# Kernel tuning notes

Hardware: AMD Instinct MI355X
Metric: run time of the kernel (lower is better)

Reference implementation:

```python
import jax, jax.numpy as jnp
import numpy as np


def _gcn_conv(x, src, dst, deg_inv_sqrt, W, b):
    # PyG GCNConv: h = x @ W; out = sum_{j->i} norm_ij * h_j  (+ bias)
    # src/dst already include self-loops; deg_inv_sqrt computed with self-loops.
    h = x @ W                                   # [N, F_out]
    norm = deg_inv_sqrt[src] * deg_inv_sqrt[dst]  # [E']
    msgs = h[src] * norm[:, None]               # [E', F_out] gather + scale
    out = jax.ops.segment_sum(msgs, dst, num_segments=x.shape[0])
    return out + b


def setup_inputs() -> dict:
    key = jax.random.key(0)
    k1, k2, k3, k4, k5 = jax.random.split(key, 5)
    N, E = 100000, 3200000
    in_c, hid, out_c = 256, 32, 128
    x = jax.random.normal(k1, (N, in_c), dtype=jnp.float32)
    edge_index = jax.random.randint(k2, (2, E), 0, N, dtype=jnp.int64)
    # Glorot-init weights, zero bias (PyG GCNConv defaults)
    W1 = jax.random.normal(k3, (in_c, hid), dtype=jnp.float32) * (2.0 / (in_c + hid)) ** 0.5
    b1 = jnp.zeros((hid,), dtype=jnp.float32)
    W2 = jax.random.normal(k4, (hid, out_c), dtype=jnp.float32) * (2.0 / (hid + out_c)) ** 0.5
    b2 = jnp.zeros((out_c,), dtype=jnp.float32)
    return {"x": x, "edge_index": edge_index, "W1": W1, "b1": b1, "W2": W2, "b2": b2}


def reference(x, edge_index, W1, b1, W2, b2):
    N = x.shape[0]
    # Add self-loops once; shared by both layers.
    loop = jnp.arange(N, dtype=edge_index.dtype)
    src = jnp.concatenate([edge_index[0], loop])
    dst = jnp.concatenate([edge_index[1], loop])
    deg = jax.ops.segment_sum(jnp.ones_like(dst, dtype=x.dtype), dst, num_segments=N)
    deg_inv_sqrt = jnp.where(deg > 0, jax.lax.rsqrt(deg), 0.0)

    h = _gcn_conv(x, src, dst, deg_inv_sqrt, W1, b1)
    h = jax.nn.relu(h)
    out = _gcn_conv(h, src, dst, deg_inv_sqrt, W2, b2)
    return out
```

## Files before the change

kernel.cpp:

```cpp
#include <hip/hip_runtime.h>

#define BSH 7
#define BNODES 128
#define SCHUNK 8192
#define MAXBUCK 800

static __device__ __forceinline__ float frelu(float v){ return v > 0.f ? v : 0.f; }

typedef __attribute__((ext_vector_type(8))) short bf16x8;
typedef __attribute__((ext_vector_type(4))) float f32x4;

static __device__ __forceinline__ unsigned short bf16_trunc(float f){
    return (unsigned short)(__builtin_bit_cast(unsigned int, f) >> 16);
}
static __device__ __forceinline__ float bf16_back(unsigned short h){
    return __builtin_bit_cast(float, ((unsigned int)h) << 16);
}

__global__ void detect_kernel(const unsigned int* __restrict__ e, int* __restrict__ flag){
    __shared__ int odd_nz;
    if (threadIdx.x == 0) odd_nz = 0;
    __syncthreads();
    int local = 0;
    for (int i = threadIdx.x; i < 512; i += blockDim.x){
        if (e[2*i + 1] != 0u) local = 1;
    }
    if (local) atomicOr(&odd_nz, 1);
    __syncthreads();
    if (threadIdx.x == 0) *flag = (odd_nz == 0) ? 1 : 0;
}

static __device__ __forceinline__ int load_idx(const void* eidx, int flg, long long pos){
    if (flg) return (int)((const long long*)eidx)[pos];
    return ((const int*)eidx)[pos];
}

__global__ void w1cvt_kernel(const float* __restrict__ W1,
        unsigned short* __restrict__ Whi, unsigned short* __restrict__ Wlo){
    int i = blockIdx.x * 256 + threadIdx.x;
    if (i < 8192){
        int k = i >> 5, c = i & 31;
        float f = W1[i];
        unsigned short h = bf16_trunc(f);
        unsigned short l = bf16_trunc(f - bf16_back(h));
        Whi[c * 256 + k] = h;
        Wlo[c * 256 + k] = l;
    }
}

__global__ __launch_bounds__(512) void buckcount_kernel(const void* __restrict__ eidx,
        const int* __restrict__ flag, int* __restrict__ bcnt, int E, int nbuck){
    __shared__ int h[MAXBUCK];
    int tid = threadIdx.x;
    int flg = *flag;
    for (int i = tid; i < nbuck; i += 512) h[i] = 0;
    __syncthreads();
    long long c0 = (long long)blockIdx.x * SCHUNK;
    int cnt = (int)min((long long)SCHUNK, (long long)E - c0);
    for (int i = tid; i < cnt; i += 512)
        atomicAdd(&h[load_idx(eidx, flg, (long long)E + c0 + i) >> BSH], 1);
    __syncthreads();
    for (int i = tid; i < nbuck; i += 512)
        if (h[i]) atomicAdd(&bcnt[i], h[i]);
}

__global__ void bucket_scan_kernel(const int* __restrict__ bcnt, int* __restrict__ boff,
                                   int* __restrict__ bcursor, int nbuck){
    __shared__ int sums[1024];
    int tid = threadIdx.x;
    int s = (tid < nbuck) ? bcnt[tid] : 0;
    sums[tid] = s;
    __syncthreads();
    for (int off = 1; off < 1024; off <<= 1){
        int t = (tid >= off) ? sums[tid - off] : 0;
        __syncthreads();
        sums[tid] += t;
        __syncthreads();
    }
    if (tid < nbuck){
        int pfx = sums[tid] - s;
        boff[tid]    = pfx;
        bcursor[tid] = pfx;
    }
    if (tid == 0) boff[nbuck] = sums[1023];
}

__global__ __launch_bounds__(512) void binned_scatter_kernel(
        const void* __restrict__ eidx, const int* __restrict__ flag,
        int* __restrict__ bcursor, unsigned int* __restrict__ bpk, int E, int nbuck){
    __shared__ int hist[MAXBUCK];
    __shared__ int base[MAXBUCK];
    __shared__ unsigned short rank[SCHUNK];
    int tid = threadIdx.x;
    int flg = *flag;
    long long c0 = (long long)blockIdx.x * SCHUNK;
    int cnt = (int)min((long long)SCHUNK, (long long)E - c0);
    for (int i = tid; i < nbuck; i += 512) hist[i] = 0;
    __syncthreads();
    for (int i = tid; i < cnt; i += 512){
        int dst = load_idx(eidx, flg, (long long)E + c0 + i);
        rank[i] = (unsigned short)atomicAdd(&hist[dst >> BSH], 1);
    }
    __syncthreads();
    for (int i = tid; i < nbuck; i += 512){
        int h = hist[i];
        base[i] = h ? atomicAdd(&bcursor[i], h) : 0;
    }
    __syncthreads();
    for (int i = tid; i < cnt; i += 512){
        int src = load_idx(eidx, flg, c0 + i);
        int dst = load_idx(eidx, flg, (long long)E + c0 + i);
        unsigned int local = (unsigned int)(dst & (BNODES - 1));
        bpk[base[dst >> BSH] + (int)rank[i]] = (local << 24) | (unsigned int)src;
    }
}

__global__ __launch_bounds__(256) void node_sort_kernel(
        const unsigned int* __restrict__ bpk, const int* __restrict__ boff,
        int* __restrict__ csr, int* __restrict__ noff, int* __restrict__ deg,
        int N, int E, int nbuck){
    __shared__ int ndeg[BNODES];
    __shared__ int nbase[BNODES];
    __shared__ int ncur[BNODES];
    int b = blockIdx.x, tid = threadIdx.x;
    int beg = boff[b], end = boff[b + 1], len = end - beg;
    int nodeBase = b << BSH;
    int nNodes = min(BNODES, N - nodeBase);
    for (int i = tid; i < BNODES; i += 256) ndeg[i] = 0;
    __syncthreads();
    for (int i = tid; i < len; i += 256)
        atomicAdd(&ndeg[bpk[beg + i] >> 24], 1);
    __syncthreads();
    if (tid == 0){
        int r = beg;
        for (int l = 0; l < BNODES; ++l){ nbase[l] = r; ncur[l] = r; r += ndeg[l]; }
    }
    __syncthreads();
    for (int i = tid; i < nNodes; i += 256){
        deg[nodeBase + i]  = ndeg[i];
        noff[nodeBase + i] = nbase[i];
    }
    if (b == nbuck - 1 && tid == 0) noff[N] = E;
    for (int i = tid; i < len; i += 256){
        unsigned int p = bpk[beg + i];
        int pos = atomicAdd(&ncur[p >> 24], 1);
        csr[pos] = (int)(p & 0xFFFFFFu);
    }
}

__global__ void dis_kernel(const int* __restrict__ deg, float* __restrict__ dis, int N){
    int i = blockIdx.x * blockDim.x + threadIdx.x;
    if (i < N) dis[i] = rsqrtf((float)(deg[i] + 1));
}

__global__ __launch_bounds__(256) void gemm1_kernel(const float* __restrict__ x,
        const unsigned short* __restrict__ Whi, const unsigned short* __restrict__ Wlo,
        const float* __restrict__ dis, float* __restrict__ h1s, int N){
    int tid  = threadIdx.x;
    int lane = tid & 63;
    int wave = tid >> 6;
    int l15  = lane & 15;
    int kgrp = lane >> 4;
    int rowT = blockIdx.x * 64 + wave * 16;
    int arow = min(rowT + l15, N - 1);
    const float* xrow = x + (size_t)arow * 256;

    f32x4 acc0 = {0.f, 0.f, 0.f, 0.f};
    f32x4 acc1 = {0.f, 0.f, 0.f, 0.f};

#pragma unroll
    for (int ks = 0; ks < 8; ++ks){
        int k0 = ks * 32 + kgrp * 8;
        float4 xa = *(const float4*)(xrow + k0);
        float4 xb = *(const float4*)(xrow + k0 + 4);
        float xs[8] = {xa.x, xa.y, xa.z, xa.w, xb.x, xb.y, xb.z, xb.w};
        bf16x8 Ah, Al;
#pragma unroll
        for (int j = 0; j < 8; ++j){
            unsigned short h = bf16_trunc(xs[j]);
            Ah[j] = (short)h;
            Al[j] = (short)bf16_trunc(xs[j] - bf16_back(h));
        }
        bf16x8 Bh0 = *(const bf16x8*)(Whi + (size_t)l15 * 256 + k0);
        bf16x8 Bl0 = *(const bf16x8*)(Wlo + (size_t)l15 * 256 + k0);
        bf16x8 Bh1 = *(const bf16x8*)(Whi + (size_t)(16 + l15) * 256 + k0);
        bf16x8 Bl1 = *(const bf16x8*)(Wlo + (size_t)(16 + l15) * 256 + k0);
        acc0 = __builtin_amdgcn_mfma_f32_16x16x32_bf16(Ah, Bh0, acc0, 0, 0, 0);
        acc0 = __builtin_amdgcn_mfma_f32_16x16x32_bf16(Al, Bh0, acc0, 0, 0, 0);
        acc0 = __builtin_amdgcn_mfma_f32_16x16x32_bf16(Ah, Bl0, acc0, 0, 0, 0);
        acc0 = __builtin_amdgcn_mfma_f32_16x16x32_bf16(Al, Bl0, acc0, 0, 0, 0);
        acc1 = __builtin_amdgcn_mfma_f32_16x16x32_bf16(Ah, Bh1, acc1, 0, 0, 0);
        acc1 = __builtin_amdgcn_mfma_f32_16x16x32_bf16(Al, Bh1, acc1, 0, 0, 0);
        acc1 = __builtin_amdgcn_mfma_f32_16x16x32_bf16(Ah, Bl1, acc1, 0, 0, 0);
        acc1 = __builtin_amdgcn_mfma_f32_16x16x32_bf16(Al, Bl1, acc1, 0, 0, 0);
    }

    int r0 = rowT + kgrp * 4;
#pragma unroll
    for (int i = 0; i < 4; ++i){
        int grow = r0 + i;
        if (grow < N){
            float d = dis[grow];
            h1s[(size_t)grow * 32 + l15]      = acc0[i] * d;
            h1s[(size_t)grow * 32 + 16 + l15] = acc1[i] * d;
        }
    }
}

__global__ __launch_bounds__(256) void agg_kernel(
        const float* __restrict__ hs, const int* __restrict__ csr,
        const int* __restrict__ noff, const float* __restrict__ dis,
        const float* __restrict__ bias, float* __restrict__ outb,
        int N, int mode){
    int tid = threadIdx.x;
    int g   = blockIdx.x * 32 + (tid >> 3);
    int fq  = tid & 7;
    if (g >= N) return;
    const float4* hs4 = (const float4*)hs;
    int beg = noff[g], end = noff[g + 1];
    float4 acc = hs4[(size_t)g * 8 + fq];
    for (int k = beg; k < end; k += 8){
        int idxv = csr[k + fq];
#pragma unroll
        for (int u = 0; u < 8; ++u){
            int s = __shfl(idxv, u, 8);
            float4 v = hs4[(size_t)s * 8 + fq];
            float m = (k + u < end) ? 1.f : 0.f;
            acc.x += v.x * m; acc.y += v.y * m;
            acc.z += v.z * m; acc.w += v.w * m;
        }
    }
    float d = dis[g];
    float4 r;
    r.x = acc.x * d; r.y = acc.y * d; r.z = acc.z * d; r.w = acc.w * d;
    if (mode == 1){
        float4 bb = ((const float4*)bias)[fq];
        r.x = frelu(r.x + bb.x) * d; r.y = frelu(r.y + bb.y) * d;
        r.z = frelu(r.z + bb.z) * d; r.w = frelu(r.w + bb.w) * d;
    }
    ((float4*)outb)[(size_t)g * 8 + fq] = r;
}

__global__ __launch_bounds__(256) void gemm2_kernel(const float* __restrict__ a2,
        const float* __restrict__ W2, const float* __restrict__ b2,
        float* __restrict__ out, int N){
    int tid  = threadIdx.x;
    int colq = tid & 31;
    int rs   = tid >> 5;
    int rowT = blockIdx.x * 16 + rs * 2;

    const float4* ar[2];
#pragma unroll
    for (int r = 0; r < 2; ++r)
        ar[r] = (const float4*)(a2 + (size_t)min(rowT + r, N - 1) * 32);
    const float4* wq = (const float4*)W2 + colq;

    float acc[2][4];
#pragma unroll
    for (int r = 0; r < 2; ++r)
#pragma unroll
        for (int c = 0; c < 4; ++c) acc[r][c] = 0.f;

#pragma unroll
    for (int kc = 0; kc < 8; ++kc){
        float4 av[2], wv[4];
#pragma unroll
        for (int r = 0; r < 2; ++r) av[r] = ar[r][kc];
#pragma unroll
        for (int k = 0; k < 4; ++k) wv[k] = wq[(kc * 4 + k) * 32];
#pragma unroll
        for (int r = 0; r < 2; ++r){
            acc[r][0] += av[r].x*wv[0].x + av[r].y*wv[1].x + av[r].z*wv[2].x + av[r].w*wv[3].x;
            acc[r][1] += av[r].x*wv[0].y + av[r].y*wv[1].y + av[r].z*wv[2].y + av[r].w*wv[3].y;
            acc[r][2] += av[r].x*wv[0].z + av[r].y*wv[1].z + av[r].z*wv[2].z + av[r].w*wv[3].z;
            acc[r][3] += av[r].x*wv[0].w + av[r].y*wv[1].w + av[r].z*wv[2].w + av[r].w*wv[3].w;
        }
    }
    float4 bb = ((const float4*)b2)[colq];
#pragma unroll
    for (int r = 0; r < 2; ++r){
        int row = rowT + r;
        if (row < N){
            float4 o = make_float4(acc[r][0] + bb.x, acc[r][1] + bb.y,
                                   acc[r][2] + bb.z, acc[r][3] + bb.w);
            *(float4*)(out + (size_t)row * 128 + colq * 4) = o;
        }
    }
}

extern "C" void kernel_launch(void* const* d_in, const int* in_sizes, int n_in,
                              void* d_out, int out_size, void* d_ws, size_t ws_size,
                              hipStream_t stream){
    const float* x  = (const float*)d_in[0];
    const void*  ei = d_in[1];
    const float* W1 = (const float*)d_in[2];
    const float* b1 = (const float*)d_in[3];
    const float* W2 = (const float*)d_in[4];
    const float* b2 = (const float*)d_in[5];
    float* out = (float*)d_out;

    const int N = in_sizes[0] / 256;
    const int E = in_sizes[1] / 2;
    const int nbuck = (N + BNODES - 1) >> BSH;

    char* ws = (char*)d_ws;
    size_t off = 0;
    auto alloc = [&](size_t bytes) -> char* {
        char* p = ws + off;
        off = (off + bytes + 255) & ~(size_t)255;
        return p;
    };
    int*   flag    = (int*)  alloc(4);
    int*   bcnt    = (int*)  alloc((size_t)nbuck * 4);
    int*   boff    = (int*)  alloc((size_t)(nbuck + 1) * 4);
    int*   bcursor = (int*)  alloc((size_t)nbuck * 4);
    int*   deg     = (int*)  alloc((size_t)N * 4);
    int*   noff    = (int*)  alloc((size_t)(N + 1) * 4);
    float* dis     = (float*)alloc((size_t)N * 4);
    unsigned short* Whi = (unsigned short*)alloc(8192 * 2);
    unsigned short* Wlo = (unsigned short*)alloc(8192 * 2);
    unsigned int* bpk = (unsigned int*)alloc((size_t)E * 4);
    int*   csr     = (int*)  alloc((size_t)(E + 8) * 4);
    float* h1s     = (float*)alloc((size_t)N * 32 * 4);
    float* h2s     = (float*)alloc((size_t)N * 32 * 4);
    float* a2      = h1s;

    hipMemsetAsync(bcnt, 0, (size_t)nbuck * 4, stream);
    hipMemsetAsync(csr + E, 0, 8 * 4, stream);

    const int nchunk = (E + SCHUNK - 1) / SCHUNK;
    detect_kernel        <<<1, 256, 0, stream>>>((const unsigned int*)ei, flag);
    w1cvt_kernel         <<<32, 256, 0, stream>>>(W1, Whi, Wlo);
    buckcount_kernel     <<<nchunk, 512, 0, stream>>>(ei, flag, bcnt, E, nbuck);
    bucket_scan_kernel   <<<1, 1024, 0, stream>>>(bcnt, boff, bcursor, nbuck);
    binned_scatter_kernel<<<nchunk, 512, 0, stream>>>(ei, flag, bcursor, bpk, E, nbuck);
    node_sort_kernel     <<<nbuck, 256, 0, stream>>>(bpk, boff, csr, noff, deg, N, E, nbuck);
    dis_kernel           <<<(N + 255) / 256, 256, 0, stream>>>(deg, dis, N);

    gemm1_kernel <<<(N + 63) / 64, 256, 0, stream>>>(x, Whi, Wlo, dis, h1s, N);
    agg_kernel   <<<(N + 31) / 32, 256, 0, stream>>>(h1s, csr, noff, dis, b1, h2s, N, 1);
    agg_kernel   <<<(N + 31) / 32, 256, 0, stream>>>(h2s, csr, noff, dis, b2, a2, N, 0);
    gemm2_kernel <<<(N + 15) / 16, 256, 0, stream>>>(a2, W2, b2, out, N);
}
```

Before: 286.3 us.

## Split edge bucket scatter into two-pass super-bucket then fine-bucket radix scatter

Replaces the single-pass scatter into ~782 destination buckets with a two-level radix scatter. Edges go first into 98 super-buckets of 1024 nodes, then each super-bucket is split into 8 fine buckets. Fewer buckets per pass should make the global writes more coalesced and reduce contention on the cursor atomics. The cost is an extra read and write of the full edge array, an extra E-sized buffer, and two more kernel launches.

```diff
diff --git a/kernel.cpp b/kernel.cpp
--- a/kernel.cpp
+++ b/kernel.cpp
@@ -2,8 +2,12 @@
 
 #define BSH 7
 #define BNODES 128
+#define SUPSH 10
+#define CH1 2048
+#define CH2 2048
 #define SCHUNK 8192
 #define MAXBUCK 800
+#define MAXSUP 128
 
 static __device__ __forceinline__ float frelu(float v){ return v > 0.f ? v : 0.f; }
 
@@ -85,33 +89,76 @@
     if (tid == 0) boff[nbuck] = sums[1023];
 }
 
-__global__ __launch_bounds__(512) void binned_scatter_kernel(
+__global__ void scursor_init_kernel(const int* __restrict__ boff,
+        int* __restrict__ scursor, int nbuck, int nsup){
+    int s = threadIdx.x;
+    if (s < nsup) scursor[s] = boff[min(s * 8, nbuck)];
+}
+
+__global__ __launch_bounds__(256) void super_scatter_kernel(
         const void* __restrict__ eidx, const int* __restrict__ flag,
-        int* __restrict__ bcursor, unsigned int* __restrict__ bpk, int E, int nbuck){
-    __shared__ int hist[MAXBUCK];
-    __shared__ int base[MAXBUCK];
-    __shared__ unsigned short rank[SCHUNK];
+        int* __restrict__ scursor, unsigned int* __restrict__ bpk1, int E, int nsup){
+    __shared__ unsigned int   pkd[CH1];
+    __shared__ unsigned short rank[CH1];
+    __shared__ unsigned char  sup[CH1];
+    __shared__ int hist[MAXSUP];
+    __shared__ int base[MAXSUP];
     int tid = threadIdx.x;
     int flg = *flag;
-    long long c0 = (long long)blockIdx.x * SCHUNK;
-    int cnt = (int)min((long long)SCHUNK, (long long)E - c0);
-    for (int i = tid; i < nbuck; i += 512) hist[i] = 0;
-    __syncthreads();
-    for (int i = tid; i < cnt; i += 512){
-        int dst = load_idx(eidx, flg, (long long)E + c0 + i);
-        rank[i] = (unsigned short)atomicAdd(&hist[dst >> BSH], 1);
-    }
-    __syncthreads();
-    for (int i = tid; i < nbuck; i += 512){
-        int h = hist[i];
-        base[i] = h ? atomicAdd(&bcursor[i], h) : 0;
-    }
-    __syncthreads();
-    for (int i = tid; i < cnt; i += 512){
+    long long c0 = (long long)blockIdx.x * CH1;
+    int cnt = (int)min((long long)CH1, (long long)E - c0);
+    for (int i = tid; i < nsup; i += 256) hist[i] = 0;
+    __syncthreads();
+    for (int i = tid; i < cnt; i += 256){
         int src = load_idx(eidx, flg, c0 + i);
         int dst = load_idx(eidx, flg, (long long)E + c0 + i);
-        unsigned int local = (unsigned int)(dst & (BNODES - 1));
-        bpk[base[dst >> BSH] + (int)rank[i]] = (local << 24) | (unsigned int)src;
+        int s = dst >> SUPSH;
+        pkd[i]  = ((unsigned int)(dst & 1023) << 17) | (unsigned int)src;
+        sup[i]  = (unsigned char)s;
+        rank[i] = (unsigned short)atomicAdd(&hist[s], 1);
+    }
+    __syncthreads();
+    for (int i = tid; i < nsup; i += 256){
+        int h = hist[i];
+        base[i] = h ? atomicAdd(&scursor[i], h) : 0;
+    }
+    __syncthreads();
+    for (int i = tid; i < cnt; i += 256)
+        bpk1[base[sup[i]] + (int)rank[i]] = pkd[i];
+}
+
+__global__ __launch_bounds__(256) void fine_scatter_kernel(
+        const unsigned int* __restrict__ bpk1, const int* __restrict__ boff,
+        int* __restrict__ bcursor, unsigned int* __restrict__ bpk2, int nbuck){
+    __shared__ unsigned int   pkd[CH2];
+    __shared__ unsigned short rank[CH2];
+    __shared__ int hist[8];
+    __shared__ int base[8];
+    int s  = blockIdx.x;
+    int f0 = s * 8;
+    int sbeg = boff[min(f0, nbuck)];
+    int send = boff[min(f0 + 8, nbuck)];
+    int c0 = sbeg + blockIdx.y * CH2;
+    if (c0 >= send) return;
+    int cnt = min(CH2, send - c0);
+    int tid = threadIdx.x;
+    if (tid < 8) hist[tid] = 0;
+    __syncthreads();
+    for (int i = tid; i < cnt; i += 256){
+        unsigned int p = bpk1[c0 + i];
+        pkd[i]  = p;
+        rank[i] = (unsigned short)atomicAdd(&hist[p >> 24], 1);
+    }
+    __syncthreads();
+    if (tid < 8){
+        int h = hist[tid];
+        base[tid] = h ? atomicAdd(&bcursor[f0 + tid], h) : 0;
+    }
+    __syncthreads();
+    for (int i = tid; i < cnt; i += 256){
+        unsigned int p = pkd[i];
+        unsigned int l7 = (p >> 17) & 127u;
+        bpk2[base[p >> 24] + (int)rank[i]] = (l7 << 24) | (p & 0x1FFFFu);
     }
 }
 
@@ -302,6 +349,7 @@
     const int N = in_sizes[0] / 256;
     const int E = in_sizes[1] / 2;
     const int nbuck = (N + BNODES - 1) >> BSH;
+    const int nsup  = (N + 1023) >> SUPSH;
 
     char* ws = (char*)d_ws;
     size_t off = 0;
@@ -314,12 +362,14 @@
     int*   bcnt    = (int*)  alloc((size_t)nbuck * 4);
     int*   boff    = (int*)  alloc((size_t)(nbuck + 1) * 4);
     int*   bcursor = (int*)  alloc((size_t)nbuck * 4);
+    int*   scursor = (int*)  alloc((size_t)nsup * 4);
     int*   deg     = (int*)  alloc((size_t)N * 4);
     int*   noff    = (int*)  alloc((size_t)(N + 1) * 4);
     float* dis     = (float*)alloc((size_t)N * 4);
     unsigned short* Whi = (unsigned short*)alloc(8192 * 2);
     unsigned short* Wlo = (unsigned short*)alloc(8192 * 2);
-    unsigned int* bpk = (unsigned int*)alloc((size_t)E * 4);
+    unsigned int* bpk1 = (unsigned int*)alloc((size_t)E * 4);
+    unsigned int* bpk2 = (unsigned int*)alloc((size_t)E * 4);
     int*   csr     = (int*)  alloc((size_t)(E + 8) * 4);
     float* h1s     = (float*)alloc((size_t)N * 32 * 4);
     float* h2s     = (float*)alloc((size_t)N * 32 * 4);
@@ -328,13 +378,17 @@
     hipMemsetAsync(bcnt, 0, (size_t)nbuck * 4, stream);
     hipMemsetAsync(csr + E, 0, 8 * 4, stream);
 
-    const int nchunk = (E + SCHUNK - 1) / SCHUNK;
     detect_kernel        <<<1, 256, 0, stream>>>((const unsigned int*)ei, flag);
     w1cvt_kernel         <<<32, 256, 0, stream>>>(W1, Whi, Wlo);
-    buckcount_kernel     <<<nchunk, 512, 0, stream>>>(ei, flag, bcnt, E, nbuck);
+    buckcount_kernel     <<<(E + SCHUNK - 1) / SCHUNK, 512, 0, stream>>>(ei, flag, bcnt, E, nbuck);
     bucket_scan_kernel   <<<1, 1024, 0, stream>>>(bcnt, boff, bcursor, nbuck);
-    binned_scatter_kernel<<<nchunk, 512, 0, stream>>>(ei, flag, bcursor, bpk, E, nbuck);
-    node_sort_kernel     <<<nbuck, 256, 0, stream>>>(bpk, boff, csr, noff, deg, N, E, nbuck);
+    scursor_init_kernel  <<<1, 128, 0, stream>>>(boff, scursor, nbuck, nsup);
+    super_scatter_kernel <<<(E + CH1 - 1) / CH1, 256, 0, stream>>>(ei, flag, scursor, bpk1, E, nsup);
+    {
+        dim3 fgrid(nsup, 64);
+        fine_scatter_kernel<<<fgrid, 256, 0, stream>>>(bpk1, boff, bcursor, bpk2, nbuck);
+    }
+    node_sort_kernel     <<<nbuck, 256, 0, stream>>>(bpk2, boff, csr, noff, deg, N, E, nbuck);
     dis_kernel           <<<(N + 255) / 256, 256, 0, stream>>>(deg, dis, N);
 
     gemm1_kernel <<<(N + 63) / 64, 256, 0, stream>>>(x, Whi, Wlo, dis, h1s, N);
```

After: 306.2 us. 1.07x slower.
